# Kernel optimization log

Hardware: AMD Instinct MI355X
Metric: run time of the kernel (lower is better)

## Reference

```python
import jax, jax.numpy as jnp
import numpy as np

B, N, E, T, M = 8, 1024, 128, 16, 256  # batch, nodes, channels, time points, modes


def setup_inputs() -> dict:
    key = jax.random.key(0)
    k1, k2, k3 = jax.random.split(key, 3)
    x = jax.random.normal(k1, (B, N, E), dtype=jnp.float32)
    # identical, sorted, strictly-positive time grids per batch element
    times = jnp.tile((jnp.arange(T, dtype=jnp.float32) + 1.0) / T, (B, 1))
    # graph Fourier basis: orthonormal eigenvector matrices per graph
    A = np.asarray(jax.random.normal(k2, (B, N, N), dtype=jnp.float32))
    U_batch = jnp.asarray(np.linalg.qr(A)[0].astype(np.float32))
    # ODEFunction_real weights: scale * rand(modes1, in_ch, out_ch)
    W = (1.0 / (E * E)) * jax.random.uniform(k3, (M, E, E), dtype=jnp.float32)
    return {"x": x, "times": times, "U_batch": U_batch, "W": W}


def _ode_func(y, W):
    # y: [M, B, E] ; W: [M, E, E] -> per-mode channel mixing
    return jnp.einsum('mbe,mef->mbf', y, W)


def _rk4_step(y, h, W):
    # torchdiffeq 'rk4' fixed-grid step (3/8 rule, autonomous RHS)
    third = 1.0 / 3.0
    k1 = _ode_func(y, W)
    k2 = _ode_func(y + h * third * k1, W)
    k3 = _ode_func(y + h * (k2 - third * k1), W)
    k4 = _ode_func(y + h * (k1 - k2 + k3), W)
    return y + h * (k1 + 3.0 * k2 + 3.0 * k3 + k4) * 0.125


def _forward(x, times, U_batch, W):
    # graph Fourier transform: x_hat[b] = U[b]^T @ x[b]
    x_hat = jnp.einsum('bin,bie->bne', U_batch, x)          # [B, N, E]
    x_ft = jnp.swapaxes(x_hat, 0, 1)[:M]                     # [M, B, E]

    # unique time points (static size T; all rows share the same grid)
    t_union, inv = jnp.unique(times.ravel(), size=T, return_inverse=True)
    indices = inv.reshape(B, T)                              # [B, T]
    ts = jnp.concatenate([jnp.zeros((1,), times.dtype), t_union])
    hs = jnp.diff(ts)                                        # [T]

    def step(y, h):
        y1 = _rk4_step(y, h, W)
        return y1, y1

    _, sol = jax.lax.scan(step, x_ft, hs)                    # [T, M, B, E]
    arr = sol.transpose(2, 0, 1, 3)                          # [B, L=T, M, E]
    desired = jnp.take_along_axis(arr, indices[:, :, None, None], axis=1)  # [B, T, M, E]

    # inverse graph Fourier transform (zero-padding M->N == using first M columns of U)
    x_pred = jnp.einsum('bnm,btme->btne', U_batch[:, :, :M], desired)       # [B, T, N, E]
    return jnp.swapaxes(x_pred, 0, 1)                        # [T, B, N, E]


def reference(x, times, U_batch, W):
    return _forward(x, times, U_batch, W)
```

## Files before the change

kernel.cpp:

```cpp
#include <hip/hip_runtime.h>

#define B_ 8
#define N_ 1024
#define E_ 128
#define T_ 16
#define M_ 256

#define UT_STRIDE 1088
#define UB_STRIDE 272

typedef __attribute__((ext_vector_type(8))) short bf16x8;
typedef __attribute__((ext_vector_type(4))) float f32x4;

__device__ __forceinline__ unsigned short f32_to_bf16_rn(float f) {
  unsigned u = __float_as_uint(f);
  u = (u + 0x7fffu + ((u >> 16) & 1u)) >> 16;
  return (unsigned short)u;
}

__global__ __launch_bounds__(256) void kprep_U(const float* __restrict__ U,
                                               unsigned short* __restrict__ Ubf,
                                               unsigned short* __restrict__ Ut) {
  __shared__ unsigned short L[64 * 72];
  const int m0 = blockIdx.x * 64, n0 = blockIdx.y * 64, b = blockIdx.z;
  const int t = threadIdx.x;
  const int r = t >> 2, c16 = (t & 3) * 16;
  const float* src = U + ((size_t)(b * N_ + n0 + r)) * N_ + m0 + c16;
  unsigned wbuf[8];
#pragma unroll
  for (int u = 0; u < 4; ++u) {
    const float4 v = ((const float4*)src)[u];
    wbuf[2 * u + 0] = (unsigned)f32_to_bf16_rn(v.x) | ((unsigned)f32_to_bf16_rn(v.y) << 16);
    wbuf[2 * u + 1] = (unsigned)f32_to_bf16_rn(v.z) | ((unsigned)f32_to_bf16_rn(v.w) << 16);
  }
  *(uint4*)&L[r * 72 + c16] = make_uint4(wbuf[0], wbuf[1], wbuf[2], wbuf[3]);
  *(uint4*)&L[r * 72 + c16 + 8] = make_uint4(wbuf[4], wbuf[5], wbuf[6], wbuf[7]);
  unsigned short* dA = Ubf + ((size_t)(b * N_ + n0 + r)) * UB_STRIDE + m0 + c16;
  *(uint4*)&dA[0] = make_uint4(wbuf[0], wbuf[1], wbuf[2], wbuf[3]);
  *(uint4*)&dA[8] = make_uint4(wbuf[4], wbuf[5], wbuf[6], wbuf[7]);
  __syncthreads();
  const int mrow = t >> 2, nq = (t & 3) * 16;
  unsigned ow[8];
#pragma unroll
  for (int i = 0; i < 8; ++i) {
    const unsigned lo = L[(nq + 2 * i) * 72 + mrow];
    const unsigned hi = L[(nq + 2 * i + 1) * 72 + mrow];
    ow[i] = lo | (hi << 16);
  }
  unsigned short* dT = Ut + ((size_t)(b * M_ + m0 + mrow)) * UT_STRIDE + n0 + nq;
  *(uint4*)&dT[0] = make_uint4(ow[0], ow[1], ow[2], ow[3]);
  *(uint4*)&dT[8] = make_uint4(ow[4], ow[5], ow[6], ow[7]);
}

__global__ __launch_bounds__(256) void kprep_x(const float* __restrict__ x,
                                               unsigned short* __restrict__ xt) {
  __shared__ unsigned short L[64 * 72];
  const int e0 = blockIdx.x * 64, i0 = blockIdx.y * 64, b = blockIdx.z;
  const int t = threadIdx.x;
  const int r = t >> 2, c16 = (t & 3) * 16;
  const float* src = x + ((size_t)(b * N_ + i0 + r)) * E_ + e0 + c16;
  unsigned wbuf[8];
#pragma unroll
  for (int u = 0; u < 4; ++u) {
    const float4 v = ((const float4*)src)[u];
    wbuf[2 * u + 0] = (unsigned)f32_to_bf16_rn(v.x) | ((unsigned)f32_to_bf16_rn(v.y) << 16);
    wbuf[2 * u + 1] = (unsigned)f32_to_bf16_rn(v.z) | ((unsigned)f32_to_bf16_rn(v.w) << 16);
  }
  *(uint4*)&L[r * 72 + c16] = make_uint4(wbuf[0], wbuf[1], wbuf[2], wbuf[3]);
  *(uint4*)&L[r * 72 + c16 + 8] = make_uint4(wbuf[4], wbuf[5], wbuf[6], wbuf[7]);
  __syncthreads();
  const int erow = t >> 2, iq = (t & 3) * 16;
  unsigned ow[8];
#pragma unroll
  for (int i = 0; i < 8; ++i) {
    const unsigned lo = L[(iq + 2 * i) * 72 + erow];
    const unsigned hi = L[(iq + 2 * i + 1) * 72 + erow];
    ow[i] = lo | (hi << 16);
  }
  unsigned short* dT = xt + ((size_t)(b * E_ + e0 + erow)) * UT_STRIDE + i0 + iq;
  *(uint4*)&dT[0] = make_uint4(ow[0], ow[1], ow[2], ow[3]);
  *(uint4*)&dT[8] = make_uint4(ow[4], ow[5], ow[6], ow[7]);
}

__global__ __launch_bounds__(256) void k1_gft(const unsigned short* __restrict__ Ut,
                                              const unsigned short* __restrict__ xt,
                                              float* __restrict__ xftp) {
  __shared__ unsigned short As[64 * 72];
  __shared__ unsigned short Bs[128 * 72];
  const int mt = blockIdx.x, b = blockIdx.y, ks = blockIdx.z;
  const int m0 = mt * 64, i0 = ks * 64;
  const int tid = threadIdx.x, lane = tid & 63, w = tid >> 6;
  const int quad = lane >> 4, ln15 = lane & 15;
  {
    const int m = tid >> 2, kq = (tid & 3) * 16;
    const unsigned short* s = Ut + ((size_t)(b * M_ + m0 + m)) * UT_STRIDE + i0 + kq;
    *(uint4*)&As[m * 72 + kq] = *(const uint4*)&s[0];
    *(uint4*)&As[m * 72 + kq + 8] = *(const uint4*)&s[8];
  }
  {
    const int e = tid >> 1, kq = (tid & 1) * 32;
    const unsigned short* s = xt + ((size_t)(b * E_ + e)) * UT_STRIDE + i0 + kq;
#pragma unroll
    for (int u = 0; u < 4; ++u)
      *(uint4*)&Bs[e * 72 + kq + u * 8] = *(const uint4*)&s[u * 8];
  }
  __syncthreads();
  f32x4 acc[8];
#pragma unroll
  for (int j = 0; j < 8; ++j) acc[j] = (f32x4){0.f, 0.f, 0.f, 0.f};
#pragma unroll
  for (int kc = 0; kc < 2; ++kc) {
    const bf16x8 aF = *(const bf16x8*)&As[(w * 16 + ln15) * 72 + kc * 32 + quad * 8];
#pragma unroll
    for (int j = 0; j < 8; ++j) {
      const bf16x8 bF = *(const bf16x8*)&Bs[(16 * j + ln15) * 72 + kc * 32 + quad * 8];
      acc[j] = __builtin_amdgcn_mfma_f32_16x16x32_bf16(aF, bF, acc[j], 0, 0, 0);
    }
  }
  float* dst = xftp + ((size_t)(ks * M_ + m0 + w * 16) * B_ + b) * E_;
#pragma unroll
  for (int j = 0; j < 8; ++j)
#pragma unroll
    for (int r = 0; r < 4; ++r)
      dst[(size_t)(quad * 4 + r) * (B_ * E_) + 16 * j + ln15] = acc[j][r];
}

__global__ __launch_bounds__(256) void k_pbuild(const float* __restrict__ W,
                                                unsigned short* __restrict__ PgT) {
  __shared__ unsigned short bufPrev[128 * 128];
  __shared__ unsigned short bufHT[128 * 128];
  const int m = blockIdx.x, tid = threadIdx.x;
  const int lane = tid & 63, w = tid >> 6;
  const int quad = lane >> 4, ln15 = lane & 15;
  const float* Wm = W + (size_t)m * 16384;
  const float h = 1.f / 16.f;
#pragma unroll
  for (int v = 0; v < 16; ++v) {
    const int idx = (v * 256 + tid) * 4;
    const float4 val = *(const float4*)&Wm[idx];
    const int k = idx >> 7, c = idx & 127;
    const unsigned short h0 = f32_to_bf16_rn(val.x * h);
    const unsigned short h1 = f32_to_bf16_rn(val.y * h);
    const unsigned short h2 = f32_to_bf16_rn(val.z * h);
    const unsigned short h3 = f32_to_bf16_rn(val.w * h);
    *(uint2*)&bufPrev[idx] =
        make_uint2((unsigned)h0 | ((unsigned)h1 << 16), (unsigned)h2 | ((unsigned)h3 << 16));
    bufHT[(c + 0) * 128 + k] = h0;
    bufHT[(c + 1) * 128 + k] = h1;
    bufHT[(c + 2) * 128 + k] = h2;
    bufHT[(c + 3) * 128 + k] = h3;
  }
  __syncthreads();
  const int rbase = w * 32;
  f32x4 Pacc[2][8];
#pragma unroll
  for (int i = 0; i < 2; ++i)
#pragma unroll
    for (int j = 0; j < 8; ++j) Pacc[i][j] = (f32x4){0.f, 0.f, 0.f, 0.f};
  const float coef[3] = {0.5f, 1.f / 6.f, 1.f / 24.f};
  for (int g = 0; g < 3; ++g) {
    f32x4 C[2][8];
#pragma unroll
    for (int i = 0; i < 2; ++i)
#pragma unroll
      for (int j = 0; j < 8; ++j) C[i][j] = (f32x4){0.f, 0.f, 0.f, 0.f};
#pragma unroll
    for (int kc = 0; kc < 128; kc += 32) {
      bf16x8 aF[2], bF[8];
#pragma unroll
      for (int i = 0; i < 2; ++i)
        aF[i] = *(const bf16x8*)&bufPrev[(rbase + 16 * i + ln15) * 128 + kc + quad * 8];
#pragma unroll
      for (int j = 0; j < 8; ++j)
        bF[j] = *(const bf16x8*)&bufHT[(16 * j + ln15) * 128 + kc + quad * 8];
#pragma unroll
      for (int i = 0; i < 2; ++i)
#pragma unroll
        for (int j = 0; j < 8; ++j)
          C[i][j] = __builtin_amdgcn_mfma_f32_16x16x32_bf16(aF[i], bF[j], C[i][j], 0, 0, 0);
    }
#pragma unroll
    for (int i = 0; i < 2; ++i)
#pragma unroll
      for (int j = 0; j < 8; ++j)
#pragma unroll
        for (int r = 0; r < 4; ++r) Pacc[i][j][r] += coef[g] * C[i][j][r];
    if (g < 2) {
      __syncthreads();
#pragma unroll
      for (int i = 0; i < 2; ++i)
#pragma unroll
        for (int j = 0; j < 8; ++j)
#pragma unroll
          for (int r = 0; r < 4; ++r) {
            const int row = rbase + 16 * i + quad * 4 + r;
            const int col = 16 * j + ln15;
            bufPrev[row * 128 + col] = f32_to_bf16_rn(C[i][j][r]);
          }
      __syncthreads();
    }
  }
  __syncthreads();
#pragma unroll
  for (int i = 0; i < 2; ++i)
#pragma unroll
    for (int j = 0; j < 8; ++j)
#pragma unroll
      for (int r = 0; r < 4; ++r) {
        const int row = rbase + 16 * i + quad * 4 + r;
        const int col = 16 * j + ln15;
        const float v = Pacc[i][j][r] + h * Wm[row * 128 + col] + (row == col ? 1.f : 0.f);
        bufHT[col * 128 + row] = f32_to_bf16_rn(v);
      }
  __syncthreads();
  unsigned short* Pm = PgT + (size_t)m * 16384;
#pragma unroll
  for (int v = 0; v < 8; ++v) {
    const int o = (v * 256 + tid) * 8;
    *(uint4*)&Pm[o] = *(const uint4*)&bufHT[o];
  }
}

__global__ __launch_bounds__(256) void k2_ode(const float* __restrict__ xftp,
                                              const unsigned short* __restrict__ PgT,
                                              unsigned short* __restrict__ Y) {
  __shared__ unsigned short Pt[128 * 128];
  __shared__ unsigned short ztb[2 * 16 * 136];
  const int m = blockIdx.x, tid = threadIdx.x;
  const int lane = tid & 63, w = tid >> 6, quad = lane >> 4, ln15 = lane & 15;
  const unsigned short* Pm = PgT + (size_t)m * 16384;
#pragma unroll
  for (int v = 0; v < 8; ++v) {
    const int idx = (v * 256 + tid) * 8;
    *(uint4*)&Pt[idx] = *(const uint4*)&Pm[idx];
  }
  {
    const int b = tid >> 5, e0 = (tid & 31) * 4;
    float4 a = make_float4(0.f, 0.f, 0.f, 0.f);
#pragma unroll
    for (int ks = 0; ks < 16; ++ks) {
      const float4 v = *(const float4*)&xftp[(((size_t)ks * M_ + m) * B_ + b) * E_ + e0];
      a.x += v.x; a.y += v.y; a.z += v.z; a.w += v.w;
    }
    const unsigned short q0 = f32_to_bf16_rn(a.x), q1 = f32_to_bf16_rn(a.y);
    const unsigned short q2 = f32_to_bf16_rn(a.z), q3 = f32_to_bf16_rn(a.w);
    *(uint2*)&ztb[b * 136 + e0] =
        make_uint2((unsigned)q0 | ((unsigned)q1 << 16), (unsigned)q2 | ((unsigned)q3 << 16));
    for (int idx = 8 * 136 + tid; idx < 16 * 136; idx += 256) ztb[idx] = 0;
  }
  __syncthreads();
  bf16x8 Bf[2][4];
#pragma unroll
  for (int nt = 0; nt < 2; ++nt)
#pragma unroll
    for (int c4 = 0; c4 < 4; ++c4)
      Bf[nt][c4] = *(const bf16x8*)&Pt[(w * 32 + nt * 16 + ln15) * 128 + c4 * 32 + quad * 8];

  int p = 0;
  for (int t = 0; t < T_; ++t) {
    const unsigned short* zr = &ztb[p * 2176];
    unsigned short* zw = &ztb[(1 - p) * 2176];
    bf16x8 aF[4];
#pragma unroll
    for (int c4 = 0; c4 < 4; ++c4)
      aF[c4] = *(const bf16x8*)&zr[ln15 * 136 + c4 * 32 + quad * 8];
    f32x4 acc[2];
    acc[0] = (f32x4){0.f, 0.f, 0.f, 0.f};
    acc[1] = (f32x4){0.f, 0.f, 0.f, 0.f};
#pragma unroll
    for (int c4 = 0; c4 < 4; ++c4) {
      acc[0] = __builtin_amdgcn_mfma_f32_16x16x32_bf16(aF[c4], Bf[0][c4], acc[0], 0, 0, 0);
      acc[1] = __builtin_amdgcn_mfma_f32_16x16x32_bf16(aF[c4], Bf[1][c4], acc[1], 0, 0, 0);
    }
#pragma unroll
    for (int nt = 0; nt < 2; ++nt)
#pragma unroll
      for (int r = 0; r < 4; ++r) {
        const int row = quad * 4 + r;
        const int e = w * 32 + nt * 16 + ln15;
        const unsigned short hv = f32_to_bf16_rn(acc[nt][r]);
        zw[row * 136 + e] = hv;
        if (row < 8) Y[(((size_t)row * M_ + m) << 11) + (t << 7) + e] = hv;
      }
    __syncthreads();
    p ^= 1;
  }
}

__global__ __launch_bounds__(256) void k_transY(const unsigned short* __restrict__ Y,
                                                unsigned short* __restrict__ Yt) {
  __shared__ unsigned short L[64 * 72];
  const int te0 = blockIdx.x * 64, m0 = blockIdx.y * 64, b = blockIdx.z;
  const int tid = threadIdx.x;
#pragma unroll
  for (int p = 0; p < 2; ++p) {
    const int r = (tid >> 3) + p * 32, tq = (tid & 7) * 8;
    const uint4 v = *(const uint4*)&Y[(((size_t)b * M_ + m0 + r) << 11) + te0 + tq];
    *(uint4*)&L[r * 72 + tq] = v;
  }
  __syncthreads();
#pragma unroll
  for (int p = 0; p < 2; ++p) {
    const int tr = (tid >> 3) + p * 32, mq = (tid & 7) * 8;
    unsigned short tmp[8];
#pragma unroll
    for (int i = 0; i < 8; ++i) tmp[i] = L[(mq + i) * 72 + tr];
    *(uint4*)&Yt[((size_t)(b * 2048) + te0 + tr) * UB_STRIDE + m0 + mq] = *(const uint4*)tmp;
  }
}

__global__ __launch_bounds__(256) void k3_igft(const unsigned short* __restrict__ Ubf,
                                               const unsigned short* __restrict__ Yt,
                                               float* __restrict__ out) {
  __shared__ __align__(16) char smem[2 * 128 * 72 * 2];
  unsigned short* As = (unsigned short*)smem;
  unsigned short* Bs = (unsigned short*)(smem + 18432);
  float* Cst = (float*)smem;
  const int tt = blockIdx.x, nb = blockIdx.y, b = blockIdx.z;
  const int n0 = nb * 128;
  const int tid = threadIdx.x, lane = tid & 63, w = tid >> 6;
  const int quad = lane >> 4, ln15 = lane & 15;
  const int hn = w >> 1, hv = w & 1;
  const unsigned short* Ua = Ubf + ((size_t)b * N_ + n0) * UB_STRIDE;
  const unsigned short* Ya = Yt + ((size_t)(b * 2048) + tt * 128) * UB_STRIDE;
  f32x4 acc[4][4];
#pragma unroll
  for (int i = 0; i < 4; ++i)
#pragma unroll
    for (int j = 0; j < 4; ++j) acc[i][j] = (f32x4){0.f, 0.f, 0.f, 0.f};
  for (int kc = 0; kc < 256; kc += 64) {
    __syncthreads();
#pragma unroll
    for (int p = 0; p < 4; ++p) {
      const int f = p * 256 + tid;
      const int r = f >> 3, u8 = (f & 7) * 8;
      *(uint4*)&As[r * 72 + u8] = *(const uint4*)&Ua[(size_t)r * UB_STRIDE + kc + u8];
      *(uint4*)&Bs[r * 72 + u8] = *(const uint4*)&Ya[(size_t)r * UB_STRIDE + kc + u8];
    }
    __syncthreads();
#pragma unroll
    for (int kc2 = 0; kc2 < 2; ++kc2) {
      bf16x8 aF[4], bF[4];
#pragma unroll
      for (int i = 0; i < 4; ++i)
        aF[i] = *(const bf16x8*)&As[(hn * 64 + 16 * i + ln15) * 72 + kc2 * 32 + quad * 8];
#pragma unroll
      for (int j = 0; j < 4; ++j)
        bF[j] = *(const bf16x8*)&Bs[(hv * 64 + 16 * j + ln15) * 72 + kc2 * 32 + quad * 8];
#pragma unroll
      for (int i = 0; i < 4; ++i)
#pragma unroll
        for (int j = 0; j < 4; ++j)
          acc[i][j] = __builtin_amdgcn_mfma_f32_16x16x32_bf16(aF[i], bF[j], acc[i][j], 0, 0, 0);
    }
  }
  float* ob = out + ((size_t)tt * B_ + b) * N_ * E_ + (size_t)n0 * E_;
#pragma unroll
  for (int c = 0; c < 4; ++c) {
    __syncthreads();
    if (hn == (c >> 1)) {
#pragma unroll
      for (int ii = 0; ii < 2; ++ii) {
        const int i = 2 * (c & 1) + ii;
#pragma unroll
        for (int j = 0; j < 4; ++j)
#pragma unroll
          for (int r = 0; r < 4; ++r)
            Cst[(16 * ii + quad * 4 + r) * 132 + hv * 64 + 16 * j + ln15] = acc[i][j][r];
      }
    }
    __syncthreads();
#pragma unroll
    for (int v = 0; v < 4; ++v) {
      const int f = v * 256 + tid;
      const int lr = f >> 5, e4 = (f & 31) * 4;
      *(float4*)&ob[(size_t)(c * 32 + lr) * E_ + e4] = *(const float4*)&Cst[lr * 132 + e4];
    }
  }
}

extern "C" void kernel_launch(void* const* d_in, const int* in_sizes, int n_in,
                              void* d_out, int out_size, void* d_ws, size_t ws_size,
                              hipStream_t stream) {
  const float* x = (const float*)d_in[0];
  const float* U = (const float*)d_in[2];
  const float* W = (const float*)d_in[3];
  float* out = (float*)d_out;

  char* ws = (char*)d_ws;
  float* xftp = (float*)ws;
  unsigned short* PgT = (unsigned short*)(ws + (16u << 20));
  unsigned short* Y = (unsigned short*)(ws + (24u << 20));
  unsigned short* Ut = (unsigned short*)(ws + (32u << 20));
  unsigned short* xt = (unsigned short*)(ws + (40u << 20));
  unsigned short* Ubf = (unsigned short*)(ws + (44u << 20));
  unsigned short* Yt = (unsigned short*)(ws + (52u << 20));

  kprep_U<<<dim3(4, 16, B_), 256, 0, stream>>>(U, Ubf, Ut);
  kprep_x<<<dim3(2, 16, B_), 256, 0, stream>>>(x, xt);
  k_pbuild<<<dim3(M_), 256, 0, stream>>>(W, PgT);
  k1_gft<<<dim3(4, B_, 16), 256, 0, stream>>>(Ut, xt, xftp);
  k2_ode<<<dim3(M_), 256, 0, stream>>>(xftp, PgT, Y);
  k_transY<<<dim3(32, 4, B_), 256, 0, stream>>>(Y, Yt);
  k3_igft<<<dim3(16, 8, B_), 256, 0, stream>>>(Ubf, Yt, out);
}
```

Before: 168.8 us.

## Merge prep kernels into one launch and fold Y transpose into igft loads

Combines the U, x and propagator-build preprocessing kernels into a single launch, with the block index selecting the role. It also removes the separate Y transpose kernel: k3_igft now reads Y in its native layout and transposes it into an XOR-swizzled shared tile while loading. Shared buffers for the propagator use a padded stride to reduce LDS bank conflicts. This cuts two launches and one global round trip of Y. In exchange, the igft B-tile load becomes scalar LDS stores, and the merged prep kernel carries the pbuild kernel's larger shared memory on every block, which may lower occupancy.

```diff
diff --git a/kernel.cpp b/kernel.cpp
--- a/kernel.cpp
+++ b/kernel.cpp
@@ -8,6 +8,7 @@
 
 #define UT_STRIDE 1088
 #define UB_STRIDE 272
+#define PP 136
 
 typedef __attribute__((ext_vector_type(8))) short bf16x8;
 typedef __attribute__((ext_vector_type(4))) float f32x4;
@@ -18,68 +19,154 @@
   return (unsigned short)u;
 }
 
-__global__ __launch_bounds__(256) void kprep_U(const float* __restrict__ U,
-                                               unsigned short* __restrict__ Ubf,
-                                               unsigned short* __restrict__ Ut) {
-  __shared__ unsigned short L[64 * 72];
-  const int m0 = blockIdx.x * 64, n0 = blockIdx.y * 64, b = blockIdx.z;
-  const int t = threadIdx.x;
-  const int r = t >> 2, c16 = (t & 3) * 16;
-  const float* src = U + ((size_t)(b * N_ + n0 + r)) * N_ + m0 + c16;
-  unsigned wbuf[8];
-#pragma unroll
-  for (int u = 0; u < 4; ++u) {
-    const float4 v = ((const float4*)src)[u];
-    wbuf[2 * u + 0] = (unsigned)f32_to_bf16_rn(v.x) | ((unsigned)f32_to_bf16_rn(v.y) << 16);
-    wbuf[2 * u + 1] = (unsigned)f32_to_bf16_rn(v.z) | ((unsigned)f32_to_bf16_rn(v.w) << 16);
-  }
-  *(uint4*)&L[r * 72 + c16] = make_uint4(wbuf[0], wbuf[1], wbuf[2], wbuf[3]);
-  *(uint4*)&L[r * 72 + c16 + 8] = make_uint4(wbuf[4], wbuf[5], wbuf[6], wbuf[7]);
-  unsigned short* dA = Ubf + ((size_t)(b * N_ + n0 + r)) * UB_STRIDE + m0 + c16;
-  *(uint4*)&dA[0] = make_uint4(wbuf[0], wbuf[1], wbuf[2], wbuf[3]);
-  *(uint4*)&dA[8] = make_uint4(wbuf[4], wbuf[5], wbuf[6], wbuf[7]);
-  __syncthreads();
-  const int mrow = t >> 2, nq = (t & 3) * 16;
-  unsigned ow[8];
-#pragma unroll
-  for (int i = 0; i < 8; ++i) {
-    const unsigned lo = L[(nq + 2 * i) * 72 + mrow];
-    const unsigned hi = L[(nq + 2 * i + 1) * 72 + mrow];
-    ow[i] = lo | (hi << 16);
-  }
-  unsigned short* dT = Ut + ((size_t)(b * M_ + m0 + mrow)) * UT_STRIDE + n0 + nq;
-  *(uint4*)&dT[0] = make_uint4(ow[0], ow[1], ow[2], ow[3]);
-  *(uint4*)&dT[8] = make_uint4(ow[4], ow[5], ow[6], ow[7]);
-}
-
-__global__ __launch_bounds__(256) void kprep_x(const float* __restrict__ x,
-                                               unsigned short* __restrict__ xt) {
-  __shared__ unsigned short L[64 * 72];
-  const int e0 = blockIdx.x * 64, i0 = blockIdx.y * 64, b = blockIdx.z;
-  const int t = threadIdx.x;
-  const int r = t >> 2, c16 = (t & 3) * 16;
-  const float* src = x + ((size_t)(b * N_ + i0 + r)) * E_ + e0 + c16;
-  unsigned wbuf[8];
-#pragma unroll
-  for (int u = 0; u < 4; ++u) {
-    const float4 v = ((const float4*)src)[u];
-    wbuf[2 * u + 0] = (unsigned)f32_to_bf16_rn(v.x) | ((unsigned)f32_to_bf16_rn(v.y) << 16);
-    wbuf[2 * u + 1] = (unsigned)f32_to_bf16_rn(v.z) | ((unsigned)f32_to_bf16_rn(v.w) << 16);
-  }
-  *(uint4*)&L[r * 72 + c16] = make_uint4(wbuf[0], wbuf[1], wbuf[2], wbuf[3]);
-  *(uint4*)&L[r * 72 + c16 + 8] = make_uint4(wbuf[4], wbuf[5], wbuf[6], wbuf[7]);
-  __syncthreads();
-  const int erow = t >> 2, iq = (t & 3) * 16;
-  unsigned ow[8];
-#pragma unroll
-  for (int i = 0; i < 8; ++i) {
-    const unsigned lo = L[(iq + 2 * i) * 72 + erow];
-    const unsigned hi = L[(iq + 2 * i + 1) * 72 + erow];
-    ow[i] = lo | (hi << 16);
-  }
-  unsigned short* dT = xt + ((size_t)(b * E_ + e0 + erow)) * UT_STRIDE + i0 + iq;
-  *(uint4*)&dT[0] = make_uint4(ow[0], ow[1], ow[2], ow[3]);
-  *(uint4*)&dT[8] = make_uint4(ow[4], ow[5], ow[6], ow[7]);
+__global__ __launch_bounds__(256) void kprep(const float* __restrict__ U,
+                                             const float* __restrict__ x,
+                                             const float* __restrict__ W,
+                                             unsigned short* __restrict__ Ubf,
+                                             unsigned short* __restrict__ Ut,
+                                             unsigned short* __restrict__ xt,
+                                             unsigned short* __restrict__ PgT) {
+  __shared__ __align__(16) unsigned short S[2 * 128 * PP];
+  const int bid = blockIdx.x, t = threadIdx.x;
+
+  if (bid < 768) {
+    unsigned short* L = S;
+    const int r = t >> 2, c16 = (t & 3) * 16;
+    const float* src;
+    unsigned short* dA = nullptr;
+    unsigned short* dTbase;
+    if (bid < 512) {
+      const int m0 = (bid & 3) * 64, n0 = ((bid >> 2) & 15) * 64, b = bid >> 6;
+      src = U + ((size_t)(b * N_ + n0 + r)) * N_ + m0 + c16;
+      dA = Ubf + ((size_t)(b * N_ + n0 + r)) * UB_STRIDE + m0 + c16;
+      dTbase = Ut + ((size_t)(b * M_ + m0)) * UT_STRIDE + n0;
+    } else {
+      const int u = bid - 512;
+      const int e0 = (u & 1) * 64, i0 = ((u >> 1) & 15) * 64, b = u >> 5;
+      src = x + ((size_t)(b * N_ + i0 + r)) * E_ + e0 + c16;
+      dTbase = xt + ((size_t)(b * E_ + e0)) * UT_STRIDE + i0;
+    }
+    unsigned wbuf[8];
+#pragma unroll
+    for (int u = 0; u < 4; ++u) {
+      const float4 v = ((const float4*)src)[u];
+      wbuf[2 * u + 0] = (unsigned)f32_to_bf16_rn(v.x) | ((unsigned)f32_to_bf16_rn(v.y) << 16);
+      wbuf[2 * u + 1] = (unsigned)f32_to_bf16_rn(v.z) | ((unsigned)f32_to_bf16_rn(v.w) << 16);
+    }
+    *(uint4*)&L[r * 72 + c16] = make_uint4(wbuf[0], wbuf[1], wbuf[2], wbuf[3]);
+    *(uint4*)&L[r * 72 + c16 + 8] = make_uint4(wbuf[4], wbuf[5], wbuf[6], wbuf[7]);
+    if (dA) {
+      *(uint4*)&dA[0] = make_uint4(wbuf[0], wbuf[1], wbuf[2], wbuf[3]);
+      *(uint4*)&dA[8] = make_uint4(wbuf[4], wbuf[5], wbuf[6], wbuf[7]);
+    }
+    __syncthreads();
+    const int q = (t & 3) * 16;
+    unsigned ow[8];
+#pragma unroll
+    for (int i = 0; i < 8; ++i) {
+      const unsigned lo = L[(q + 2 * i) * 72 + r];
+      const unsigned hi = L[(q + 2 * i + 1) * 72 + r];
+      ow[i] = lo | (hi << 16);
+    }
+    unsigned short* dT = dTbase + (size_t)r * UT_STRIDE + q;
+    *(uint4*)&dT[0] = make_uint4(ow[0], ow[1], ow[2], ow[3]);
+    *(uint4*)&dT[8] = make_uint4(ow[4], ow[5], ow[6], ow[7]);
+    return;
+  }
+
+  const int m = bid - 768;
+  unsigned short* bufPrev = S;
+  unsigned short* bufHT = S + 128 * PP;
+  const int lane = t & 63, w = t >> 6;
+  const int quad = lane >> 4, ln15 = lane & 15;
+  const float* Wm = W + (size_t)m * 16384;
+  const float h = 1.f / 16.f;
+#pragma unroll
+  for (int v = 0; v < 16; ++v) {
+    const int idx = (v * 256 + t) * 4;
+    const float4 val = *(const float4*)&Wm[idx];
+    const int k = idx >> 7, c = idx & 127;
+    const unsigned short h0 = f32_to_bf16_rn(val.x * h);
+    const unsigned short h1 = f32_to_bf16_rn(val.y * h);
+    const unsigned short h2 = f32_to_bf16_rn(val.z * h);
+    const unsigned short h3 = f32_to_bf16_rn(val.w * h);
+    *(uint2*)&bufPrev[k * PP + c] =
+        make_uint2((unsigned)h0 | ((unsigned)h1 << 16), (unsigned)h2 | ((unsigned)h3 << 16));
+    bufHT[(c + 0) * PP + k] = h0;
+    bufHT[(c + 1) * PP + k] = h1;
+    bufHT[(c + 2) * PP + k] = h2;
+    bufHT[(c + 3) * PP + k] = h3;
+  }
+  __syncthreads();
+  const int rbase = w * 32;
+  f32x4 Pacc[2][8];
+#pragma unroll
+  for (int i = 0; i < 2; ++i)
+#pragma unroll
+    for (int j = 0; j < 8; ++j) Pacc[i][j] = (f32x4){0.f, 0.f, 0.f, 0.f};
+  const float coef[3] = {0.5f, 1.f / 6.f, 1.f / 24.f};
+  for (int g = 0; g < 3; ++g) {
+    f32x4 C[2][8];
+#pragma unroll
+    for (int i = 0; i < 2; ++i)
+#pragma unroll
+      for (int j = 0; j < 8; ++j) C[i][j] = (f32x4){0.f, 0.f, 0.f, 0.f};
+#pragma unroll
+    for (int kc = 0; kc < 128; kc += 32) {
+      bf16x8 aF[2], bF[8];
+#pragma unroll
+      for (int i = 0; i < 2; ++i)
+        aF[i] = *(const bf16x8*)&bufPrev[(rbase + 16 * i + ln15) * PP + kc + quad * 8];
+#pragma unroll
+      for (int j = 0; j < 8; ++j)
+        bF[j] = *(const bf16x8*)&bufHT[(16 * j + ln15) * PP + kc + quad * 8];
+#pragma unroll
+      for (int i = 0; i < 2; ++i)
+#pragma unroll
+        for (int j = 0; j < 8; ++j)
+          C[i][j] = __builtin_amdgcn_mfma_f32_16x16x32_bf16(aF[i], bF[j], C[i][j], 0, 0, 0);
+    }
+#pragma unroll
+    for (int i = 0; i < 2; ++i)
+#pragma unroll
+      for (int j = 0; j < 8; ++j)
+#pragma unroll
+        for (int r = 0; r < 4; ++r) Pacc[i][j][r] += coef[g] * C[i][j][r];
+    if (g < 2) {
+      __syncthreads();
+#pragma unroll
+      for (int i = 0; i < 2; ++i)
+#pragma unroll
+        for (int j = 0; j < 8; ++j)
+#pragma unroll
+          for (int r = 0; r < 4; ++r) {
+            const int row = rbase + 16 * i + quad * 4 + r;
+            const int col = 16 * j + ln15;
+            bufPrev[row * PP + col] = f32_to_bf16_rn(C[i][j][r]);
+          }
+      __syncthreads();
+    }
+  }
+  __syncthreads();
+#pragma unroll
+  for (int i = 0; i < 2; ++i)
+#pragma unroll
+    for (int j = 0; j < 8; ++j)
+#pragma unroll
+      for (int r = 0; r < 4; ++r) {
+        const int row = rbase + 16 * i + quad * 4 + r;
+        const int col = 16 * j + ln15;
+        const float v = Pacc[i][j][r] + h * Wm[row * 128 + col] + (row == col ? 1.f : 0.f);
+        bufHT[col * PP + row] = f32_to_bf16_rn(v);
+      }
+  __syncthreads();
+  unsigned short* Pm = PgT + (size_t)m * 16384;
+#pragma unroll
+  for (int v = 0; v < 8; ++v) {
+    const int idx = (v * 256 + t) * 8;
+    const int f = idx >> 7, e = idx & 127;
+    *(uint4*)&Pm[idx] = *(const uint4*)&bufHT[f * PP + e];
+  }
 }
 
 __global__ __launch_bounds__(256) void k1_gft(const unsigned short* __restrict__ Ut,
@@ -125,106 +212,10 @@
       dst[(size_t)(quad * 4 + r) * (B_ * E_) + 16 * j + ln15] = acc[j][r];
 }
 
-__global__ __launch_bounds__(256) void k_pbuild(const float* __restrict__ W,
-                                                unsigned short* __restrict__ PgT) {
-  __shared__ unsigned short bufPrev[128 * 128];
-  __shared__ unsigned short bufHT[128 * 128];
-  const int m = blockIdx.x, tid = threadIdx.x;
-  const int lane = tid & 63, w = tid >> 6;
-  const int quad = lane >> 4, ln15 = lane & 15;
-  const float* Wm = W + (size_t)m * 16384;
-  const float h = 1.f / 16.f;
-#pragma unroll
-  for (int v = 0; v < 16; ++v) {
-    const int idx = (v * 256 + tid) * 4;
-    const float4 val = *(const float4*)&Wm[idx];
-    const int k = idx >> 7, c = idx & 127;
-    const unsigned short h0 = f32_to_bf16_rn(val.x * h);
-    const unsigned short h1 = f32_to_bf16_rn(val.y * h);
-    const unsigned short h2 = f32_to_bf16_rn(val.z * h);
-    const unsigned short h3 = f32_to_bf16_rn(val.w * h);
-    *(uint2*)&bufPrev[idx] =
-        make_uint2((unsigned)h0 | ((unsigned)h1 << 16), (unsigned)h2 | ((unsigned)h3 << 16));
-    bufHT[(c + 0) * 128 + k] = h0;
-    bufHT[(c + 1) * 128 + k] = h1;
-    bufHT[(c + 2) * 128 + k] = h2;
-    bufHT[(c + 3) * 128 + k] = h3;
-  }
-  __syncthreads();
-  const int rbase = w * 32;
-  f32x4 Pacc[2][8];
-#pragma unroll
-  for (int i = 0; i < 2; ++i)
-#pragma unroll
-    for (int j = 0; j < 8; ++j) Pacc[i][j] = (f32x4){0.f, 0.f, 0.f, 0.f};
-  const float coef[3] = {0.5f, 1.f / 6.f, 1.f / 24.f};
-  for (int g = 0; g < 3; ++g) {
-    f32x4 C[2][8];
-#pragma unroll
-    for (int i = 0; i < 2; ++i)
-#pragma unroll
-      for (int j = 0; j < 8; ++j) C[i][j] = (f32x4){0.f, 0.f, 0.f, 0.f};
-#pragma unroll
-    for (int kc = 0; kc < 128; kc += 32) {
-      bf16x8 aF[2], bF[8];
-#pragma unroll
-      for (int i = 0; i < 2; ++i)
-        aF[i] = *(const bf16x8*)&bufPrev[(rbase + 16 * i + ln15) * 128 + kc + quad * 8];
-#pragma unroll
-      for (int j = 0; j < 8; ++j)
-        bF[j] = *(const bf16x8*)&bufHT[(16 * j + ln15) * 128 + kc + quad * 8];
-#pragma unroll
-      for (int i = 0; i < 2; ++i)
-#pragma unroll
-        for (int j = 0; j < 8; ++j)
-          C[i][j] = __builtin_amdgcn_mfma_f32_16x16x32_bf16(aF[i], bF[j], C[i][j], 0, 0, 0);
-    }
-#pragma unroll
-    for (int i = 0; i < 2; ++i)
-#pragma unroll
-      for (int j = 0; j < 8; ++j)
-#pragma unroll
-        for (int r = 0; r < 4; ++r) Pacc[i][j][r] += coef[g] * C[i][j][r];
-    if (g < 2) {
-      __syncthreads();
-#pragma unroll
-      for (int i = 0; i < 2; ++i)
-#pragma unroll
-        for (int j = 0; j < 8; ++j)
-#pragma unroll
-          for (int r = 0; r < 4; ++r) {
-            const int row = rbase + 16 * i + quad * 4 + r;
-            const int col = 16 * j + ln15;
-            bufPrev[row * 128 + col] = f32_to_bf16_rn(C[i][j][r]);
-          }
-      __syncthreads();
-    }
-  }
-  __syncthreads();
-#pragma unroll
-  for (int i = 0; i < 2; ++i)
-#pragma unroll
-    for (int j = 0; j < 8; ++j)
-#pragma unroll
-      for (int r = 0; r < 4; ++r) {
-        const int row = rbase + 16 * i + quad * 4 + r;
-        const int col = 16 * j + ln15;
-        const float v = Pacc[i][j][r] + h * Wm[row * 128 + col] + (row == col ? 1.f : 0.f);
-        bufHT[col * 128 + row] = f32_to_bf16_rn(v);
-      }
-  __syncthreads();
-  unsigned short* Pm = PgT + (size_t)m * 16384;
-#pragma unroll
-  for (int v = 0; v < 8; ++v) {
-    const int o = (v * 256 + tid) * 8;
-    *(uint4*)&Pm[o] = *(const uint4*)&bufHT[o];
-  }
-}
-
 __global__ __launch_bounds__(256) void k2_ode(const float* __restrict__ xftp,
                                               const unsigned short* __restrict__ PgT,
                                               unsigned short* __restrict__ Y) {
-  __shared__ unsigned short Pt[128 * 128];
+  __shared__ unsigned short Pt[128 * PP];
   __shared__ unsigned short ztb[2 * 16 * 136];
   const int m = blockIdx.x, tid = threadIdx.x;
   const int lane = tid & 63, w = tid >> 6, quad = lane >> 4, ln15 = lane & 15;
@@ -232,7 +223,8 @@
 #pragma unroll
   for (int v = 0; v < 8; ++v) {
     const int idx = (v * 256 + tid) * 8;
-    *(uint4*)&Pt[idx] = *(const uint4*)&Pm[idx];
+    const int f = idx >> 7, e = idx & 127;
+    *(uint4*)&Pt[f * PP + e] = *(const uint4*)&Pm[idx];
   }
   {
     const int b = tid >> 5, e0 = (tid & 31) * 4;
@@ -254,7 +246,7 @@
   for (int nt = 0; nt < 2; ++nt)
 #pragma unroll
     for (int c4 = 0; c4 < 4; ++c4)
-      Bf[nt][c4] = *(const bf16x8*)&Pt[(w * 32 + nt * 16 + ln15) * 128 + c4 * 32 + quad * 8];
+      Bf[nt][c4] = *(const bf16x8*)&Pt[(w * 32 + nt * 16 + ln15) * PP + c4 * 32 + quad * 8];
 
   int p = 0;
   for (int t = 0; t < T_; ++t) {
@@ -287,32 +279,10 @@
   }
 }
 
-__global__ __launch_bounds__(256) void k_transY(const unsigned short* __restrict__ Y,
-                                                unsigned short* __restrict__ Yt) {
-  __shared__ unsigned short L[64 * 72];
-  const int te0 = blockIdx.x * 64, m0 = blockIdx.y * 64, b = blockIdx.z;
-  const int tid = threadIdx.x;
-#pragma unroll
-  for (int p = 0; p < 2; ++p) {
-    const int r = (tid >> 3) + p * 32, tq = (tid & 7) * 8;
-    const uint4 v = *(const uint4*)&Y[(((size_t)b * M_ + m0 + r) << 11) + te0 + tq];
-    *(uint4*)&L[r * 72 + tq] = v;
-  }
-  __syncthreads();
-#pragma unroll
-  for (int p = 0; p < 2; ++p) {
-    const int tr = (tid >> 3) + p * 32, mq = (tid & 7) * 8;
-    unsigned short tmp[8];
-#pragma unroll
-    for (int i = 0; i < 8; ++i) tmp[i] = L[(mq + i) * 72 + tr];
-    *(uint4*)&Yt[((size_t)(b * 2048) + te0 + tr) * UB_STRIDE + m0 + mq] = *(const uint4*)tmp;
-  }
-}
-
 __global__ __launch_bounds__(256) void k3_igft(const unsigned short* __restrict__ Ubf,
-                                               const unsigned short* __restrict__ Yt,
+                                               const unsigned short* __restrict__ Y,
                                                float* __restrict__ out) {
-  __shared__ __align__(16) char smem[2 * 128 * 72 * 2];
+  __shared__ __align__(16) char smem[18432 + 16384];
   unsigned short* As = (unsigned short*)smem;
   unsigned short* Bs = (unsigned short*)(smem + 18432);
   float* Cst = (float*)smem;
@@ -322,7 +292,7 @@
   const int quad = lane >> 4, ln15 = lane & 15;
   const int hn = w >> 1, hv = w & 1;
   const unsigned short* Ua = Ubf + ((size_t)b * N_ + n0) * UB_STRIDE;
-  const unsigned short* Ya = Yt + ((size_t)(b * 2048) + tt * 128) * UB_STRIDE;
+  const unsigned short* Ym = Y + ((size_t)b * M_) * 2048 + tt * 128;
   f32x4 acc[4][4];
 #pragma unroll
   for (int i = 0; i < 4; ++i)
@@ -335,7 +305,21 @@
       const int f = p * 256 + tid;
       const int r = f >> 3, u8 = (f & 7) * 8;
       *(uint4*)&As[r * 72 + u8] = *(const uint4*)&Ua[(size_t)r * UB_STRIDE + kc + u8];
-      *(uint4*)&Bs[r * 72 + u8] = *(const uint4*)&Ya[(size_t)r * UB_STRIDE + kc + u8];
+    }
+#pragma unroll
+    for (int p = 0; p < 4; ++p) {
+      const int f = p * 256 + tid;
+      const int ml = f >> 4;
+      const int te8 = (f & 15) * 8;
+      const uint4 v = *(const uint4*)&Ym[(size_t)(kc + ml) * 2048 + te8];
+      const unsigned short* sv = (const unsigned short*)&v;
+      const int kb = ml >> 3, klo = ml & 7;
+#pragma unroll
+      for (int i = 0; i < 8; ++i) {
+        const int te = te8 + i;
+        const int blk = kb ^ ((te >> 3) & 7);
+        Bs[te * 64 + blk * 8 + klo] = sv[i];
+      }
     }
     __syncthreads();
 #pragma unroll
@@ -345,8 +329,11 @@
       for (int i = 0; i < 4; ++i)
         aF[i] = *(const bf16x8*)&As[(hn * 64 + 16 * i + ln15) * 72 + kc2 * 32 + quad * 8];
 #pragma unroll
-      for (int j = 0; j < 4; ++j)
-        bF[j] = *(const bf16x8*)&Bs[(hv * 64 + 16 * j + ln15) * 72 + kc2 * 32 + quad * 8];
+      for (int j = 0; j < 4; ++j) {
+        const int row = hv * 64 + 16 * j + ln15;
+        const int blk = (kc2 * 4 + quad) ^ ((row >> 3) & 7);
+        bF[j] = *(const bf16x8*)&Bs[row * 64 + blk * 8];
+      }
 #pragma unroll
       for (int i = 0; i < 4; ++i)
 #pragma unroll
@@ -394,13 +381,9 @@
   unsigned short* Ut = (unsigned short*)(ws + (32u << 20));
   unsigned short* xt = (unsigned short*)(ws + (40u << 20));
   unsigned short* Ubf = (unsigned short*)(ws + (44u << 20));
-  unsigned short* Yt = (unsigned short*)(ws + (52u << 20));
-
-  kprep_U<<<dim3(4, 16, B_), 256, 0, stream>>>(U, Ubf, Ut);
-  kprep_x<<<dim3(2, 16, B_), 256, 0, stream>>>(x, xt);
-  k_pbuild<<<dim3(M_), 256, 0, stream>>>(W, PgT);
+
+  kprep<<<dim3(1024), 256, 0, stream>>>(U, x, W, Ubf, Ut, xt, PgT);
   k1_gft<<<dim3(4, B_, 16), 256, 0, stream>>>(Ut, xt, xftp);
   k2_ode<<<dim3(M_), 256, 0, stream>>>(xftp, PgT, Y);
-  k_transY<<<dim3(32, 4, B_), 256, 0, stream>>>(Y, Yt);
-  k3_igft<<<dim3(16, 8, B_), 256, 0, stream>>>(Ubf, Yt, out);
-}
+  k3_igft<<<dim3(16, 8, B_), 256, 0, stream>>>(Ubf, Y, out);
+}
```

After: 159.5 us. 5.5% less time.
